# Performance work log

Measured on AMD Instinct MI355X. Metric: run time of the kernel, lower is better.

Reference implementation:

```python
import jax, jax.numpy as jnp
import numpy as np

B, T, C = 2, 1024, 768
H, NE, K = 3072, 8, 2


def setup_inputs() -> dict:
    key = jax.random.key(0)
    k1, k2, k3, k4 = jax.random.split(key, 4)
    x = jax.random.normal(k1, (B, T, C), dtype=jnp.float32)
    w_fc = jax.random.normal(k2, (C, H * NE), dtype=jnp.float32) * 0.02
    w_proj = jax.random.normal(k3, (H * NE, C), dtype=jnp.float32) * (0.02 * (2 * 12) ** -0.5)
    w_gate = jax.random.normal(k4, (C, NE), dtype=jnp.float32) * 0.02
    return {"x": x, "w_fc": w_fc, "w_proj": w_proj, "w_gate": w_gate}


def reference(x, w_fc, w_proj, w_gate):
    # Router: softmax over experts, top-k, renormalize selected probs.
    router_logits = jnp.einsum('btc,ce->bte', x, w_gate)
    router_probs = jax.nn.softmax(router_logits, axis=-1)
    top_p, top_i = jax.lax.top_k(router_probs, K)          # (B,T,K)
    top_p = top_p / jnp.sum(top_p, axis=-1, keepdims=True)

    # First projection. Original gathers (C,H,B,T,K) weight slices then
    # einsum('btc,chbtk->bthk'); mathematically identical to projecting with
    # all experts and gathering the selected outputs (same contraction order).
    wf = w_fc.reshape(C, H, NE)
    h_all = jnp.einsum('btc,che->bthe', x, wf)             # (B,T,H,NE)
    h = jnp.take_along_axis(h_all, top_i[:, :, None, :], axis=-1)  # (B,T,H,K)
    h = jax.nn.gelu(h, approximate=True)

    # Second projection + weighted combine over the K selected experts.
    wp = w_proj.reshape(H, C, NE)
    o_all = jnp.einsum('bthk,hce->btcke', h, wp)           # (B,T,C,K,NE)
    o = jnp.take_along_axis(o_all, top_i[:, :, None, :, None], axis=-1)[..., 0]  # (B,T,C,K)
    o = jnp.einsum('btck,btk->btc', o, top_p)
    return o
```

## Files before the change

kernel.cpp:

```cpp
#include <hip/hip_runtime.h>
#include <hip/hip_bf16.h>
#include <math.h>

#define BB 2
#define TT 1024
#define CC 768
#define HH 3072
#define NEXP 8
#define NTOK (BB*TT)
#define CAP 1024
#define CNT_STRIDE 32

typedef __attribute__((ext_vector_type(8))) short short8;
typedef __attribute__((ext_vector_type(4))) float float4v;

typedef const __attribute__((address_space(1))) void* gptr_t;
typedef __attribute__((address_space(3))) void* sptr_t;

__device__ __forceinline__ unsigned short f2bf(float f) {
    unsigned int u = __float_as_uint(f);
    unsigned int r = (u + 0x7fffu + ((u >> 16) & 1u)) >> 16;
    return (unsigned short)r;
}
__device__ __forceinline__ float gelu_tanh(float v) {
    const float k2 = 2.0f * 0.7978845608028654f;
    const float k1 = 0.044715f;
    float z = k2 * (v + k1 * v * v * v);
    return v / (1.0f + __expf(-z));
}

__global__ void router_kernel(const float* __restrict__ x,
                              const float* __restrict__ w_gate,
                              float* __restrict__ top_p,
                              int* __restrict__ counts,
                              int* __restrict__ tok_list) {
    int t = blockIdx.x;
    int lane = threadIdx.x;
    float acc[NEXP];
#pragma unroll
    for (int e = 0; e < NEXP; ++e) acc[e] = 0.f;
    for (int c = lane; c < CC; c += 64) {
        float xv = x[t * CC + c];
        const float4* wg = (const float4*)(w_gate + c * NEXP);
        float4 w0 = wg[0], w1 = wg[1];
        acc[0] += xv * w0.x; acc[1] += xv * w0.y;
        acc[2] += xv * w0.z; acc[3] += xv * w0.w;
        acc[4] += xv * w1.x; acc[5] += xv * w1.y;
        acc[6] += xv * w1.z; acc[7] += xv * w1.w;
    }
#pragma unroll
    for (int e = 0; e < NEXP; ++e) {
        for (int off = 32; off > 0; off >>= 1)
            acc[e] += __shfl_down(acc[e], off, 64);
    }
    if (lane == 0) {
        float m = acc[0];
#pragma unroll
        for (int e = 1; e < NEXP; ++e) m = fmaxf(m, acc[e]);
        float p[NEXP]; float s = 0.f;
#pragma unroll
        for (int e = 0; e < NEXP; ++e) { p[e] = expf(acc[e] - m); s += p[e]; }
        float inv_s = 1.f / s;
#pragma unroll
        for (int e = 0; e < NEXP; ++e) p[e] *= inv_s;
        int i0 = 0;
#pragma unroll
        for (int e = 1; e < NEXP; ++e) if (p[e] > p[i0]) i0 = e;
        int i1 = (i0 == 0) ? 1 : 0;
#pragma unroll
        for (int e = 0; e < NEXP; ++e) if (e != i0 && p[e] > p[i1]) i1 = e;
        float p0 = p[i0], p1 = p[i1];
        float inv = 1.f / (p0 + p1);
        top_p[t * 2 + 0] = p0 * inv;
        top_p[t * 2 + 1] = p1 * inv;
        int pos0 = atomicAdd(&counts[i0 * CNT_STRIDE], 1);
        if (pos0 < CAP) tok_list[i0 * NTOK + pos0] = t * 2 + 0;
        int pos1 = atomicAdd(&counts[i1 * CNT_STRIDE], 1);
        if (pos1 < CAP) tok_list[i1 * NTOK + pos1] = t * 2 + 1;
    }
}

__global__ __launch_bounds__(256)
void permute_w(const float* __restrict__ In, unsigned short* __restrict__ Out,
               int Adim, int Bdim) {
    __shared__ unsigned short L[32 * 256];
    int a0 = blockIdx.x * 32, b0 = blockIdx.y * 32;
    int t = threadIdx.x;
#pragma unroll
    for (int j = 0; j < 8; ++j) {
        int idx = j * 256 + t;
        int ar = idx >> 6;
        int wi = idx & 63;
        const float4 v = *(const float4*)(In + (size_t)(a0 + ar) * Bdim * 8 + b0 * 8 + wi * 4);
        ushort4 s;
        s.x = f2bf(v.x); s.y = f2bf(v.y); s.z = f2bf(v.z); s.w = f2bf(v.w);
        *(ushort4*)&L[ar * 256 + wi * 4] = s;
    }
    __syncthreads();
    unsigned short tmp[32];
#pragma unroll
    for (int a = 0; a < 32; ++a) tmp[a] = L[a * 256 + t];
    int b = b0 + (t >> 3), e = t & 7;
    unsigned short* dst = Out + ((size_t)e * Bdim + b) * Adim + a0;
#pragma unroll
    for (int j = 0; j < 8; ++j) {
        ushort4 s; s.x = tmp[j*4+0]; s.y = tmp[j*4+1]; s.z = tmp[j*4+2]; s.w = tmp[j*4+3];
        *(ushort4*)(dst + j * 4) = s;
    }
}

__global__ void gather_x(const float* __restrict__ x,
                         const int* __restrict__ counts,
                         const int* __restrict__ tok_list,
                         unsigned short* __restrict__ xg) {
    int pos = blockIdx.x;
    int e = pos >> 10, i = pos & (CAP - 1);
    int M = counts[e * CNT_STRIDE]; if (M > CAP) M = CAP;
    int Mr = (M + 127) & ~127; if (Mr > CAP) Mr = CAP;
    if (i >= Mr) return;
    int c = threadIdx.x * 4;
    unsigned short* dst = xg + (size_t)pos * CC + c;
    ushort4 s;
    if (i < M) {
        int tk = tok_list[e * NTOK + i] >> 1;
        float4 v = *(const float4*)(x + (size_t)tk * CC + c);
        s.x = f2bf(v.x); s.y = f2bf(v.y); s.z = f2bf(v.z); s.w = f2bf(v.w);
    } else {
        s.x = s.y = s.z = s.w = 0;
    }
    *(ushort4*)dst = s;
}

__global__ __launch_bounds__(256)
void gemm1_mfma(const unsigned short* __restrict__ xg,
                const unsigned short* __restrict__ wfc_b,
                const int* __restrict__ counts,
                unsigned short* __restrict__ h_slab) {
    int e = blockIdx.z;
    int M = counts[e * CNT_STRIDE]; if (M > CAP) M = CAP;
    int m0 = blockIdx.y * 128;
    if (m0 >= M) return;
    int n0 = blockIdx.x * 128;

    __shared__ unsigned short As[2][128 * 32];
    __shared__ unsigned short Bs[2][128 * 32];

    int tid = threadIdx.x;
    int wave = tid >> 6, lane = tid & 63;
    int wm = wave >> 1, wn = wave & 1;
    int quad = lane >> 4, l16 = lane & 15;

    const unsigned short* aBase = xg + ((size_t)e * CAP + m0) * CC;
    const unsigned short* bBase = wfc_b + ((size_t)e * HH + n0) * CC;

    int srow = wave * 32 + (lane >> 2);
    int schunk = (lane & 3) * 8;

    float4v acc[4][4];
#pragma unroll
    for (int i = 0; i < 4; ++i)
#pragma unroll
        for (int j = 0; j < 4; ++j)
#pragma unroll
            for (int r = 0; r < 4; ++r) acc[i][j][r] = 0.f;

#pragma unroll
    for (int q = 0; q < 2; ++q) {
        int r = srow + q * 16;
        __builtin_amdgcn_global_load_lds(
            (gptr_t)(aBase + (size_t)r * CC + schunk),
            (sptr_t)(&As[0][(wave * 32 + q * 16) * 32]), 16, 0, 0);
        __builtin_amdgcn_global_load_lds(
            (gptr_t)(bBase + (size_t)r * CC + schunk),
            (sptr_t)(&Bs[0][(wave * 32 + q * 16) * 32]), 16, 0, 0);
    }

    for (int k0 = 0; k0 < CC; k0 += 32) {
        int cur = (k0 >> 5) & 1;
        __syncthreads();
        if (k0 + 32 < CC) {
            int nxt = cur ^ 1;
#pragma unroll
            for (int q = 0; q < 2; ++q) {
                int r = srow + q * 16;
                __builtin_amdgcn_global_load_lds(
                    (gptr_t)(aBase + (size_t)r * CC + k0 + 32 + schunk),
                    (sptr_t)(&As[nxt][(wave * 32 + q * 16) * 32]), 16, 0, 0);
                __builtin_amdgcn_global_load_lds(
                    (gptr_t)(bBase + (size_t)r * CC + k0 + 32 + schunk),
                    (sptr_t)(&Bs[nxt][(wave * 32 + q * 16) * 32]), 16, 0, 0);
            }
        }
        short8 af[4], bf[4];
#pragma unroll
        for (int mt = 0; mt < 4; ++mt)
            af[mt] = *(const short8*)&As[cur][(wm * 64 + mt * 16 + l16) * 32 + quad * 8];
#pragma unroll
        for (int nt = 0; nt < 4; ++nt)
            bf[nt] = *(const short8*)&Bs[cur][(wn * 64 + nt * 16 + l16) * 32 + quad * 8];
#pragma unroll
        for (int mt = 0; mt < 4; ++mt)
#pragma unroll
            for (int nt = 0; nt < 4; ++nt)
                acc[mt][nt] = __builtin_amdgcn_mfma_f32_16x16x32_bf16(
                    af[mt], bf[nt], acc[mt][nt], 0, 0, 0);
    }

#pragma unroll
    for (int mt = 0; mt < 4; ++mt) {
#pragma unroll
        for (int r = 0; r < 4; ++r) {
            int m = m0 + wm * 64 + mt * 16 + quad * 4 + r;
            unsigned short* orow = h_slab + ((size_t)e * CAP + m) * HH + n0 + wn * 64 + l16;
#pragma unroll
            for (int nt = 0; nt < 4; ++nt)
                orow[nt * 16] = f2bf(gelu_tanh(acc[mt][nt][r]));
        }
    }
}

__global__ __launch_bounds__(256)
void gemm2_mfma(const unsigned short* __restrict__ h_slab,
                const unsigned short* __restrict__ wp_b,
                const int* __restrict__ counts,
                const int* __restrict__ tok_list,
                float* __restrict__ o_part) {
    int e = blockIdx.z;
    int M = counts[e * CNT_STRIDE]; if (M > CAP) M = CAP;
    int m0 = blockIdx.y * 128;
    if (m0 >= M) return;
    int n0 = (blockIdx.x >> 2) * 128;
    int ks = blockIdx.x & 3;

    __shared__ unsigned short As[2][128 * 32];
    __shared__ unsigned short Bs[2][128 * 32];

    int tid = threadIdx.x;
    int wave = tid >> 6, lane = tid & 63;
    int wm = wave >> 1, wn = wave & 1;
    int quad = lane >> 4, l16 = lane & 15;

    const unsigned short* aBase = h_slab + ((size_t)e * CAP + m0) * HH + ks * 768;
    const unsigned short* bBase = wp_b + ((size_t)e * CC + n0) * HH + ks * 768;

    int srow = wave * 32 + (lane >> 2);
    int schunk = (lane & 3) * 8;

    float4v acc[4][4];
#pragma unroll
    for (int i = 0; i < 4; ++i)
#pragma unroll
        for (int j = 0; j < 4; ++j)
#pragma unroll
            for (int r = 0; r < 4; ++r) acc[i][j][r] = 0.f;

#pragma unroll
    for (int q = 0; q < 2; ++q) {
        int r = srow + q * 16;
        __builtin_amdgcn_global_load_lds(
            (gptr_t)(aBase + (size_t)r * HH + schunk),
            (sptr_t)(&As[0][(wave * 32 + q * 16) * 32]), 16, 0, 0);
        __builtin_amdgcn_global_load_lds(
            (gptr_t)(bBase + (size_t)r * HH + schunk),
            (sptr_t)(&Bs[0][(wave * 32 + q * 16) * 32]), 16, 0, 0);
    }

    for (int k0 = 0; k0 < 768; k0 += 32) {
        int cur = (k0 >> 5) & 1;
        __syncthreads();
        if (k0 + 32 < 768) {
            int nxt = cur ^ 1;
#pragma unroll
            for (int q = 0; q < 2; ++q) {
                int r = srow + q * 16;
                __builtin_amdgcn_global_load_lds(
                    (gptr_t)(aBase + (size_t)r * HH + k0 + 32 + schunk),
                    (sptr_t)(&As[nxt][(wave * 32 + q * 16) * 32]), 16, 0, 0);
                __builtin_amdgcn_global_load_lds(
                    (gptr_t)(bBase + (size_t)r * HH + k0 + 32 + schunk),
                    (sptr_t)(&Bs[nxt][(wave * 32 + q * 16) * 32]), 16, 0, 0);
            }
        }
        short8 af[4], bf[4];
#pragma unroll
        for (int mt = 0; mt < 4; ++mt)
            af[mt] = *(const short8*)&As[cur][(wm * 64 + mt * 16 + l16) * 32 + quad * 8];
#pragma unroll
        for (int nt = 0; nt < 4; ++nt)
            bf[nt] = *(const short8*)&Bs[cur][(wn * 64 + nt * 16 + l16) * 32 + quad * 8];
#pragma unroll
        for (int mt = 0; mt < 4; ++mt)
#pragma unroll
            for (int nt = 0; nt < 4; ++nt)
                acc[mt][nt] = __builtin_amdgcn_mfma_f32_16x16x32_bf16(
                    af[mt], bf[nt], acc[mt][nt], 0, 0, 0);
    }

#pragma unroll
    for (int mt = 0; mt < 4; ++mt) {
#pragma unroll
        for (int r = 0; r < 4; ++r) {
            int m = m0 + wm * 64 + mt * 16 + quad * 4 + r;
            if (m < M) {
                int ent = tok_list[e * NTOK + m];
                float* orow = o_part + ((size_t)ks * NTOK * 2 + ent) * CC + n0 + wn * 64 + l16;
#pragma unroll
                for (int nt = 0; nt < 4; ++nt)
                    orow[nt * 16] = acc[mt][nt][r];
            }
        }
    }
}

__global__ void combine_kernel(const float* __restrict__ o_part,
                               const float* __restrict__ top_p,
                               float* __restrict__ out) {
    int idx = blockIdx.x * 256 + threadIdx.x;
    int t = idx / (CC / 4);
    int c = (idx % (CC / 4)) * 4;
    float p0 = top_p[2 * t], p1 = top_p[2 * t + 1];
    float4 s0 = make_float4(0.f, 0.f, 0.f, 0.f);
    float4 s1 = make_float4(0.f, 0.f, 0.f, 0.f);
#pragma unroll
    for (int ks = 0; ks < 4; ++ks) {
        const float4 a = *(const float4*)(o_part + ((size_t)ks * NTOK * 2 + 2 * t) * CC + c);
        const float4 b = *(const float4*)(o_part + ((size_t)ks * NTOK * 2 + 2 * t + 1) * CC + c);
        s0.x += a.x; s0.y += a.y; s0.z += a.z; s0.w += a.w;
        s1.x += b.x; s1.y += b.y; s1.z += b.z; s1.w += b.w;
    }
    float4 r;
    r.x = p0 * s0.x + p1 * s1.x;
    r.y = p0 * s0.y + p1 * s1.y;
    r.z = p0 * s0.z + p1 * s1.z;
    r.w = p0 * s0.w + p1 * s1.w;
    *(float4*)(out + (size_t)t * CC + c) = r;
}

extern "C" void kernel_launch(void* const* d_in, const int* in_sizes, int n_in,
                              void* d_out, int out_size, void* d_ws, size_t ws_size,
                              hipStream_t stream) {
    const float* x      = (const float*)d_in[0];
    const float* w_fc   = (const float*)d_in[1];
    const float* w_proj = (const float*)d_in[2];
    const float* w_gate = (const float*)d_in[3];
    float* out = (float*)d_out;

    char* ws = (char*)d_ws;
    size_t off = 0;
    float* top_p    = (float*)(ws + off); off += NTOK * 2 * sizeof(float);
    int*   counts   = (int*)(ws + off);   off += CNT_STRIDE * NEXP * 4;
    int*   tok_list = (int*)(ws + off);   off += (size_t)NEXP * NTOK * 4;
    off = 131072;
    unsigned short* wp_b   = (unsigned short*)(ws + off); off += (size_t)NEXP*CC*HH*2;
    unsigned short* h_slab = (unsigned short*)(ws + off); off += (size_t)NEXP*CAP*HH*2;
    unsigned short* wfc_b  = (unsigned short*)(ws + off);
    float*          o_part = (float*)(ws + off);          off += (size_t)NEXP*HH*CC*2;
    unsigned short* xg     = (unsigned short*)(ws + off); off += (size_t)NEXP*CAP*CC*2;

    hipMemsetAsync(counts, 0, CNT_STRIDE * NEXP * 4, stream);

    router_kernel<<<NTOK, 64, 0, stream>>>(x, w_gate, top_p, counts, tok_list);
    permute_w<<<dim3(CC / 32, HH / 32), 256, 0, stream>>>(w_fc, wfc_b, CC, HH);
    permute_w<<<dim3(HH / 32, CC / 32), 256, 0, stream>>>(w_proj, wp_b, HH, CC);
    gather_x<<<NEXP * CAP, 192, 0, stream>>>(x, counts, tok_list, xg);

    gemm1_mfma<<<dim3(HH / 128, CAP / 128, NEXP), 256, 0, stream>>>(
        xg, wfc_b, counts, h_slab);
    gemm2_mfma<<<dim3((CC / 128) * 4, CAP / 128, NEXP), 256, 0, stream>>>(
        h_slab, wp_b, counts, tok_list, o_part);
    combine_kernel<<<(NTOK * CC / 4) / 256, 256, 0, stream>>>(o_part, top_p, out);
}
```

Before: 312.9 us.

## XOR-swizzle GEMM LDS tiles and restructure weight permute for wide stores

Both MFMA GEMMs now XOR-swizzle the 16-byte chunk position inside each 32-element LDS row, on the global-to-LDS load side and on the fragment read side, to reduce LDS bank conflicts when reading A/B fragments. The weight permute kernel is retiled to 128x8 blocks with a padded LDS row stride of 66, so each thread writes 16-byte short8 outputs instead of 8-byte ones. The aim is fewer LDS conflicts and wider global stores in the bf16 weight conversion. Correctness depends on the swizzle on the load side matching the swizzle on the read side.

```diff
diff --git a/kernel.cpp b/kernel.cpp
--- a/kernel.cpp
+++ b/kernel.cpp
@@ -83,29 +83,33 @@
 __global__ __launch_bounds__(256)
 void permute_w(const float* __restrict__ In, unsigned short* __restrict__ Out,
                int Adim, int Bdim) {
-    __shared__ unsigned short L[32 * 256];
-    int a0 = blockIdx.x * 32, b0 = blockIdx.y * 32;
+    __shared__ unsigned short L[128 * 66];
+    int a0 = blockIdx.x * 128;
+    int b0 = blockIdx.y * 8;
     int t = threadIdx.x;
 #pragma unroll
     for (int j = 0; j < 8; ++j) {
         int idx = j * 256 + t;
-        int ar = idx >> 6;
-        int wi = idx & 63;
-        const float4 v = *(const float4*)(In + (size_t)(a0 + ar) * Bdim * 8 + b0 * 8 + wi * 4);
-        ushort4 s;
-        s.x = f2bf(v.x); s.y = f2bf(v.y); s.z = f2bf(v.z); s.w = f2bf(v.w);
-        *(ushort4*)&L[ar * 256 + wi * 4] = s;
+        int r = idx >> 4, c4 = idx & 15;
+        const float4 v = *(const float4*)(In + (size_t)(a0 + r) * Bdim * 8 + b0 * 8 + c4 * 4);
+        ushort2 s01, s23;
+        s01.x = f2bf(v.x); s01.y = f2bf(v.y);
+        s23.x = f2bf(v.z); s23.y = f2bf(v.w);
+        *(ushort2*)&L[r * 66 + c4 * 4]     = s01;
+        *(ushort2*)&L[r * 66 + c4 * 4 + 2] = s23;
     }
     __syncthreads();
-    unsigned short tmp[32];
-#pragma unroll
-    for (int a = 0; a < 32; ++a) tmp[a] = L[a * 256 + t];
-    int b = b0 + (t >> 3), e = t & 7;
+    int w = t >> 6, ln = t & 63;
+    int oc = w * 16 + (ln & 15);
+    int e = oc & 7, b = b0 + (oc >> 3);
     unsigned short* dst = Out + ((size_t)e * Bdim + b) * Adim + a0;
 #pragma unroll
-    for (int j = 0; j < 8; ++j) {
-        ushort4 s; s.x = tmp[j*4+0]; s.y = tmp[j*4+1]; s.z = tmp[j*4+2]; s.w = tmp[j*4+3];
-        *(ushort4*)(dst + j * 4) = s;
+    for (int p = 0; p < 4; ++p) {
+        int seg = (ln >> 4) + p * 4;
+        short8 vv;
+#pragma unroll
+        for (int k = 0; k < 8; ++k) vv[k] = (short)L[(seg * 8 + k) * 66 + oc];
+        *(short8*)(dst + seg * 8) = vv;
     }
 }
 
@@ -154,7 +158,7 @@
     const unsigned short* bBase = wfc_b + ((size_t)e * HH + n0) * CC;
 
     int srow = wave * 32 + (lane >> 2);
-    int schunk = (lane & 3) * 8;
+    int schunk = (((lane & 3) ^ ((lane >> 3) & 3)) * 8);
 
     float4v acc[4][4];
 #pragma unroll
@@ -174,6 +178,8 @@
             (gptr_t)(bBase + (size_t)r * CC + schunk),
             (sptr_t)(&Bs[0][(wave * 32 + q * 16) * 32]), 16, 0, 0);
     }
+
+    int sa = (l16 >> 1) & 3;
 
     for (int k0 = 0; k0 < CC; k0 += 32) {
         int cur = (k0 >> 5) & 1;
@@ -194,10 +200,10 @@
         short8 af[4], bf[4];
 #pragma unroll
         for (int mt = 0; mt < 4; ++mt)
-            af[mt] = *(const short8*)&As[cur][(wm * 64 + mt * 16 + l16) * 32 + quad * 8];
+            af[mt] = *(const short8*)&As[cur][(wm * 64 + mt * 16 + l16) * 32 + (quad ^ sa) * 8];
 #pragma unroll
         for (int nt = 0; nt < 4; ++nt)
-            bf[nt] = *(const short8*)&Bs[cur][(wn * 64 + nt * 16 + l16) * 32 + quad * 8];
+            bf[nt] = *(const short8*)&Bs[cur][(wn * 64 + nt * 16 + l16) * 32 + (quad ^ sa) * 8];
 #pragma unroll
         for (int mt = 0; mt < 4; ++mt)
 #pragma unroll
@@ -244,7 +250,7 @@
     const unsigned short* bBase = wp_b + ((size_t)e * CC + n0) * HH + ks * 768;
 
     int srow = wave * 32 + (lane >> 2);
-    int schunk = (lane & 3) * 8;
+    int schunk = (((lane & 3) ^ ((lane >> 3) & 3)) * 8);
 
     float4v acc[4][4];
 #pragma unroll
@@ -264,6 +270,8 @@
             (gptr_t)(bBase + (size_t)r * HH + schunk),
             (sptr_t)(&Bs[0][(wave * 32 + q * 16) * 32]), 16, 0, 0);
     }
+
+    int sa = (l16 >> 1) & 3;
 
     for (int k0 = 0; k0 < 768; k0 += 32) {
         int cur = (k0 >> 5) & 1;
@@ -284,10 +292,10 @@
         short8 af[4], bf[4];
 #pragma unroll
         for (int mt = 0; mt < 4; ++mt)
-            af[mt] = *(const short8*)&As[cur][(wm * 64 + mt * 16 + l16) * 32 + quad * 8];
+            af[mt] = *(const short8*)&As[cur][(wm * 64 + mt * 16 + l16) * 32 + (quad ^ sa) * 8];
 #pragma unroll
         for (int nt = 0; nt < 4; ++nt)
-            bf[nt] = *(const short8*)&Bs[cur][(wn * 64 + nt * 16 + l16) * 32 + quad * 8];
+            bf[nt] = *(const short8*)&Bs[cur][(wn * 64 + nt * 16 + l16) * 32 + (quad ^ sa) * 8];
 #pragma unroll
         for (int mt = 0; mt < 4; ++mt)
 #pragma unroll
@@ -360,8 +368,8 @@
     hipMemsetAsync(counts, 0, CNT_STRIDE * NEXP * 4, stream);
 
     router_kernel<<<NTOK, 64, 0, stream>>>(x, w_gate, top_p, counts, tok_list);
-    permute_w<<<dim3(CC / 32, HH / 32), 256, 0, stream>>>(w_fc, wfc_b, CC, HH);
-    permute_w<<<dim3(HH / 32, CC / 32), 256, 0, stream>>>(w_proj, wp_b, HH, CC);
+    permute_w<<<dim3(CC / 128, HH / 8), 256, 0, stream>>>(w_fc, wfc_b, CC, HH);
+    permute_w<<<dim3(HH / 128, CC / 8), 256, 0, stream>>>(w_proj, wp_b, HH, CC);
     gather_x<<<NEXP * CAP, 192, 0, stream>>>(x, counts, tok_list, xg);
 
     gemm1_mfma<<<dim3(HH / 128, CAP / 128, NEXP), 256, 0, stream>>>(
```

New measurement: 298.8 us. 1.05x faster.
